# Kernel optimization log

Hardware: AMD Instinct MI355X
Metric: run time of the kernel (lower is better)

## Reference

```python
import jax, jax.numpy as jnp
import numpy as np

USER = 100000
ITEM = 50000
N = USER + ITEM
LATDIM = 64
IMG_DIM = 1024
E_ADJ = 3_000_000
E_IMG = 1_000_000
GNN_LAYERS = 2
RIS_LAMBDA = 1.0
EPS = 1e-12


def spmm(rows, cols, vals, x):
    # sparse [N,N] @ dense [N,D] via gather + segment-sum
    return jax.ops.segment_sum(vals[:, None] * x[cols], rows, num_segments=N)


def setup_inputs() -> dict:
    key = jax.random.key(0)
    ks = jax.random.split(key, 10)
    return {
        "adj_rows": jax.random.randint(ks[0], (E_ADJ,), 0, N, dtype=jnp.int32),
        "adj_cols": jax.random.randint(ks[1], (E_ADJ,), 0, N, dtype=jnp.int32),
        "adj_vals": jax.random.uniform(ks[2], (E_ADJ,), dtype=jnp.float32),
        "img_rows": jax.random.randint(ks[3], (E_IMG,), 0, N, dtype=jnp.int32),
        "img_cols": jax.random.randint(ks[4], (E_IMG,), 0, N, dtype=jnp.int32),
        "img_vals": jax.random.uniform(ks[5], (E_IMG,), dtype=jnp.float32),
        "image_embedding": jax.random.normal(ks[6], (ITEM, IMG_DIM), dtype=jnp.float32),
        "uEmbeds": jax.random.normal(ks[7], (USER, LATDIM), dtype=jnp.float32) * 0.01,
        "iEmbeds": jax.random.normal(ks[8], (ITEM, LATDIM), dtype=jnp.float32) * 0.01,
        "W_trans": jax.random.normal(ks[9], (IMG_DIM, LATDIM), dtype=jnp.float32) * (1.0 / np.sqrt(IMG_DIM)),
        "b_trans": jnp.zeros((LATDIM,), dtype=jnp.float32),
    }


def reference(adj_rows, adj_cols, adj_vals, img_rows, img_cols, img_vals,
              image_embedding, uEmbeds, iEmbeds, W_trans, b_trans):
    # trans == 1: Linear projection of image features
    image_feats = image_embedding @ W_trans + b_trans  # [ITEM, LATDIM]

    # image_adj @ concat(u, i)
    embeds_img_adj = spmm(img_rows, img_cols, img_vals, jnp.concatenate([uEmbeds, iEmbeds], axis=0))

    # F.normalize(image_feats) along dim=1 (L2, eps=1e-12)
    nrm = jnp.linalg.norm(image_feats, axis=1, keepdims=True)
    feats_n = image_feats / jnp.maximum(nrm, EPS)

    embeds_image = spmm(adj_rows, adj_cols, adj_vals, jnp.concatenate([uEmbeds, feats_n], axis=0))
    embeds_image_ = spmm(adj_rows, adj_cols, adj_vals,
                         jnp.concatenate([embeds_image[:USER], iEmbeds], axis=0))
    embeds_image = embeds_image + embeds_image_ + RIS_LAMBDA * embeds_img_adj

    # stacked GCN layers with sum over all layer outputs (including input)
    acc = embeds_image
    cur = embeds_image
    for _ in range(GNN_LAYERS):
        cur = spmm(adj_rows, adj_cols, adj_vals, cur)
        acc = acc + cur

    return acc[:USER], acc[USER:]
```

## Files before the change

### kernel.cpp

```cpp
#include <hip/hip_runtime.h>
#include <hip/hip_fp16.h>

#define USER_N 100000
#define ITEM_N 50000
#define NN (USER_N + ITEM_N)
#define D 64
#define IMGD 1024
#define LDP 68
#define KSPLIT 4
#define KQ (IMGD / KSPLIT)

#define BUCKET_BITS 10
#define BROWS (1 << BUCKET_BITS)
#define NBUCK ((NN + BROWS - 1) >> BUCKET_BITS)
#define CHUNK 4096

typedef _Float16 v4h __attribute__((ext_vector_type(4)));
typedef _Float16 v8h __attribute__((ext_vector_type(8)));
typedef float v4f __attribute__((ext_vector_type(4)));

typedef __attribute__((address_space(1))) unsigned int GU32;
typedef __attribute__((address_space(3))) unsigned int LU32;

__global__ __launch_bounds__(256) void wt_prep(
    const float* __restrict__ W, _Float16* __restrict__ Wt16)
{
    const int id = blockIdx.x * 256 + threadIdx.x;
    if (id >= D * IMGD) return;
    const int c = id >> 10;
    const int k = id & 1023;
    Wt16[id] = (_Float16)W[(size_t)k * D + c];
}

__global__ __launch_bounds__(256) void gemm_mfma7(
    const float* __restrict__ A, const _Float16* __restrict__ Wt16,
    float* __restrict__ P0, float* __restrict__ P123)
{
    __shared__ float As[32 * KQ];
    const int t = threadIdx.x;
    const int w = t >> 6;
    const int lane = t & 63;
    const int l16 = lane & 15;
    const int g = lane >> 4;
    const int tile = blockIdx.x >> 2;
    const int ks = blockIdx.x & 3;
    const int row0 = tile * 32;
    const int kbase = ks * KQ;

#pragma unroll
    for (int i = 0; i < 8; i++) {
        const int r = w * 8 + i;
        const int grow = row0 + r;
        const int garow = grow < ITEM_N ? grow : ITEM_N - 1;
        const int xm = (r & 7) << 4;
        const char* src = reinterpret_cast<const char*>(
            A + (size_t)garow * IMGD + kbase) + ((lane * 16) ^ xm);
        __builtin_amdgcn_global_load_lds(
            (GU32*)src, (LU32*)&As[r * KQ], 16, 0, 0);
    }
    asm volatile("s_waitcnt vmcnt(0)" ::: "memory");
    __syncthreads();

    const int wr = (w >> 1) * 16;
    const int wc = (w & 1) * 32;
    const int rr = wr + l16;
    const char* rbase = reinterpret_cast<const char*>(&As[rr * KQ]);
    const int xm = (rr & 7) << 4;

    v4f acc[2] = {};
    const _Float16* wb = Wt16 + (size_t)l16 * IMGD + kbase + g * 4;

    for (int c = 0; c < KQ; c += 64) {
        const int cb = c * 4;
        const float4 f0 = *reinterpret_cast<const float4*>(rbase + ((cb + g * 16) ^ xm));
        const float4 f1 = *reinterpret_cast<const float4*>(rbase + ((cb + 64 + g * 16) ^ xm));
        const float4 f2 = *reinterpret_cast<const float4*>(rbase + ((cb + 128 + g * 16) ^ xm));
        const float4 f3 = *reinterpret_cast<const float4*>(rbase + ((cb + 192 + g * 16) ^ xm));
        union { v8h v; v4h h[2]; } af0, af1;
        {
            v4h h;
            h[0] = (_Float16)f0.x; h[1] = (_Float16)f0.y;
            h[2] = (_Float16)f0.z; h[3] = (_Float16)f0.w;
            af0.h[0] = h;
            h[0] = (_Float16)f1.x; h[1] = (_Float16)f1.y;
            h[2] = (_Float16)f1.z; h[3] = (_Float16)f1.w;
            af0.h[1] = h;
            h[0] = (_Float16)f2.x; h[1] = (_Float16)f2.y;
            h[2] = (_Float16)f2.z; h[3] = (_Float16)f2.w;
            af1.h[0] = h;
            h[0] = (_Float16)f3.x; h[1] = (_Float16)f3.y;
            h[2] = (_Float16)f3.z; h[3] = (_Float16)f3.w;
            af1.h[1] = h;
        }
#pragma unroll
        for (int n = 0; n < 2; n++) {
            const _Float16* wp = wb + (size_t)(wc + n * 16) * IMGD + c;
            union { v8h v; v4h h[2]; } bf;
            bf.h[0] = *reinterpret_cast<const v4h*>(wp);
            bf.h[1] = *reinterpret_cast<const v4h*>(wp + 16);
            acc[n] = __builtin_amdgcn_mfma_f32_16x16x32_f16(af0.v, bf.v, acc[n], 0, 0, 0);
            bf.h[0] = *reinterpret_cast<const v4h*>(wp + 32);
            bf.h[1] = *reinterpret_cast<const v4h*>(wp + 48);
            acc[n] = __builtin_amdgcn_mfma_f32_16x16x32_f16(af1.v, bf.v, acc[n], 0, 0, 0);
        }
    }
    float* Cp = (ks == 0) ? P0 : P123 + (size_t)(ks - 1) * ITEM_N * D;
#pragma unroll
    for (int n = 0; n < 2; n++) {
        const int col = wc + n * 16 + l16;
#pragma unroll
        for (int r = 0; r < 4; r++) {
            const int grow = row0 + wr + g * 4 + r;
            if (grow < ITEM_N)
                Cp[(size_t)grow * D + col] = acc[n][r];
        }
    }
}

__global__ __launch_bounds__(256) void gemm_feats32(
    const float* __restrict__ A, const float* __restrict__ W,
    const float* __restrict__ b, float* __restrict__ C)
{
    __shared__ float As[32][LDP];
    __shared__ float Ws[64][LDP];
    const int row0 = blockIdx.x * 32;
    const int t = threadIdx.x;
    const int tx = t & 15, ty = t >> 4;
    float acc[2][4] = {};

    const int lr = t >> 4;
    const int lk = (t & 15) * 4;

    for (int k0 = 0; k0 < IMGD; k0 += 64) {
#pragma unroll
        for (int i = 0; i < 2; i++) {
            const int r = lr + i * 16;
            const int grow = row0 + r;
            float4 v = make_float4(0.f, 0.f, 0.f, 0.f);
            if (grow < ITEM_N)
                v = *reinterpret_cast<const float4*>(&A[(size_t)grow * IMGD + k0 + lk]);
            *reinterpret_cast<float4*>(&As[r][lk]) = v;
        }
#pragma unroll
        for (int i = 0; i < 4; i++) {
            const int kr = lr + i * 16;
            float4 v = *reinterpret_cast<const float4*>(&W[(size_t)(k0 + kr) * D + lk]);
            *reinterpret_cast<float4*>(&Ws[kr][lk]) = v;
        }
        __syncthreads();
#pragma unroll
        for (int kb = 0; kb < 16; kb++) {
            float a_[2][4], w_[4][4];
#pragma unroll
            for (int i = 0; i < 2; i++) {
                const float4 v = *reinterpret_cast<const float4*>(&As[ty * 2 + i][kb * 4]);
                a_[i][0] = v.x; a_[i][1] = v.y; a_[i][2] = v.z; a_[i][3] = v.w;
            }
#pragma unroll
            for (int j = 0; j < 4; j++) {
                const float4 v = *reinterpret_cast<const float4*>(&Ws[kb * 4 + j][tx * 4]);
                w_[j][0] = v.x; w_[j][1] = v.y; w_[j][2] = v.z; w_[j][3] = v.w;
            }
#pragma unroll
            for (int j = 0; j < 4; j++)
#pragma unroll
                for (int i = 0; i < 2; i++)
#pragma unroll
                    for (int c = 0; c < 4; c++)
                        acc[i][c] += a_[i][j] * w_[j][c];
        }
        __syncthreads();
    }
    const float4 bias = *reinterpret_cast<const float4*>(&b[tx * 4]);
#pragma unroll
    for (int i = 0; i < 2; i++) {
        const int grow = row0 + ty * 2 + i;
        if (grow < ITEM_N) {
            float4 v;
            v.x = acc[i][0] + bias.x;
            v.y = acc[i][1] + bias.y;
            v.z = acc[i][2] + bias.z;
            v.w = acc[i][3] + bias.w;
            *reinterpret_cast<float4*>(&C[(size_t)grow * D + tx * 4]) = v;
        }
    }
}

__global__ __launch_bounds__(256) void rownorm_h4(
    const float* __restrict__ P0, const float* __restrict__ P123,
    const float* __restrict__ b, __half* __restrict__ Y, int nrows)
{
    const int gid = blockIdx.x * blockDim.x + threadIdx.x;
    const int row = gid >> 6;
    const int lane = threadIdx.x & 63;
    if (row >= nrows) return;
    const size_t idx = (size_t)row * D + lane;
    const size_t N1 = (size_t)ITEM_N * D;
    float v = P0[idx] + P123[idx] + P123[idx + N1] + P123[idx + 2 * N1] + b[lane];
    float s = v * v;
#pragma unroll
    for (int o = 32; o > 0; o >>= 1) s += __shfl_xor(s, o, 64);
    const float scale = 1.0f / fmaxf(sqrtf(s), 1e-12f);
    Y[idx] = __float2half(v * scale);
}

__global__ __launch_bounds__(256) void rownorm(float* __restrict__ X, int nrows)
{
    const int gid = blockIdx.x * blockDim.x + threadIdx.x;
    const int row = gid >> 6;
    const int lane = threadIdx.x & 63;
    if (row >= nrows) return;
    float v = X[(size_t)row * D + lane];
    float s = v * v;
#pragma unroll
    for (int o = 32; o > 0; o >>= 1) s += __shfl_xor(s, o, 64);
    const float scale = 1.0f / fmaxf(sqrtf(s), 1e-12f);
    X[(size_t)row * D + lane] = v * scale;
}

__global__ __launch_bounds__(256) void cvt_x0(
    const float* __restrict__ uE, const float* __restrict__ iE,
    __half* __restrict__ x0, __half* __restrict__ xBI)
{
    const int i = blockIdx.x * 256 + threadIdx.x;
    const int n4u = USER_N * D / 4;
    const int n4 = NN * D / 4;
    if (i >= n4) return;
    const float4 v = (i < n4u) ? reinterpret_cast<const float4*>(uE)[i]
                               : reinterpret_cast<const float4*>(iE)[i - n4u];
    union { uint2 u2; __half2 h[2]; } o;
    o.h[0] = __floats2half2_rn(v.x, v.y);
    o.h[1] = __floats2half2_rn(v.z, v.w);
    *reinterpret_cast<uint2*>(x0 + (size_t)i * 4) = o.u2;
    if (i >= n4u)
        *reinterpret_cast<uint2*>(xBI + (size_t)(i - n4u) * 4) = o.u2;
}

__global__ __launch_bounds__(256) void bucket_count(
    const int* __restrict__ rows, int nnz, int nb, int* __restrict__ histT)
{
    __shared__ int cnt[NBUCK];
    for (int i = threadIdx.x; i < NBUCK; i += 256) cnt[i] = 0;
    __syncthreads();
    const int e0 = blockIdx.x * CHUNK;
    const int e1 = min(e0 + CHUNK, nnz);
    for (int e = e0 + threadIdx.x; e < e1; e += 256)
        atomicAdd(&cnt[rows[e] >> BUCKET_BITS], 1);
    __syncthreads();
    for (int b = threadIdx.x; b < NBUCK; b += 256)
        histT[b * nb + blockIdx.x] = cnt[b];
}

__global__ __launch_bounds__(1024) void scanA(
    const int* __restrict__ cnt, int* __restrict__ excl,
    int* __restrict__ blocksums, int n)
{
    const int t = threadIdx.x;
    const int gid = blockIdx.x * 1024 + t;
    const int lane = t & 63, wid = t >> 6;
    int v = (gid < n) ? cnt[gid] : 0;
    int x = v;
#pragma unroll
    for (int o = 1; o < 64; o <<= 1) {
        int y = __shfl_up(x, o, 64);
        if (lane >= o) x += y;
    }
    __shared__ int ws[16];
    __shared__ int wo[16];
    if (lane == 63) ws[wid] = x;
    __syncthreads();
    if (t < 16) {
        int s = ws[t];
        int xx = s;
#pragma unroll
        for (int o = 1; o < 16; o <<= 1) {
            int y = __shfl_up(xx, o, 16);
            if (t >= o) xx += y;
        }
        wo[t] = xx - s;
        if (t == 15) blocksums[blockIdx.x] = xx;
    }
    __syncthreads();
    if (gid < n) excl[gid] = x - v + wo[wid];
}

__global__ __launch_bounds__(1024) void scanB(int* __restrict__ bs, int nb)
{
    const int t = threadIdx.x;
    const int lane = t & 63, wid = t >> 6;
    int v = (t < nb) ? bs[t] : 0;
    int x = v;
#pragma unroll
    for (int o = 1; o < 64; o <<= 1) {
        int y = __shfl_up(x, o, 64);
        if (lane >= o) x += y;
    }
    __shared__ int ws[16];
    __shared__ int wo[16];
    if (lane == 63) ws[wid] = x;
    __syncthreads();
    if (t < 16) {
        int s = ws[t];
        int xx = s;
#pragma unroll
        for (int o = 1; o < 16; o <<= 1) {
            int y = __shfl_up(xx, o, 16);
            if (t >= o) xx += y;
        }
        wo[t] = xx - s;
    }
    __syncthreads();
    if (t < nb) bs[t] = x - v + wo[wid];
}

__global__ __launch_bounds__(256) void scan_apply(
    int* __restrict__ excl, const int* __restrict__ bo, int n)
{
    const int gid = blockIdx.x * blockDim.x + threadIdx.x;
    if (gid < n) excl[gid] += bo[gid >> 10];
}

__global__ __launch_bounds__(256) void bucket_place(
    const int* __restrict__ rows, const int* __restrict__ cols,
    const float* __restrict__ vals, int nnz, int nb,
    const int* __restrict__ offsT, uint2* __restrict__ rec)
{
    __shared__ int cur[NBUCK];
    for (int b = threadIdx.x; b < NBUCK; b += 256)
        cur[b] = offsT[b * nb + blockIdx.x];
    __syncthreads();
    const int e0 = blockIdx.x * CHUNK;
    const int e1 = min(e0 + CHUNK, nnz);
    for (int e = e0 + threadIdx.x; e < e1; e += 256) {
        const int r = rows[e];
        const int b = r >> BUCKET_BITS;
        const int pos = atomicAdd(&cur[b], 1);
        rec[pos] = make_uint2(((unsigned)cols[e] << BUCKET_BITS) |
                                  (unsigned)(r & (BROWS - 1)),
                              __float_as_uint(vals[e]));
    }
}

__global__ __launch_bounds__(1024) void bucket_finalize(
    const uint2* __restrict__ rec, int nnz, int nb,
    const int* __restrict__ offsT, int* __restrict__ rp,
    int2* __restrict__ ev)
{
    const int b = blockIdx.x;
    const int t = threadIdx.x;
    const int rlo = b << BUCKET_BITS;
    const int segs = offsT[b * nb];
    const int sege = (b + 1 < NBUCK) ? offsT[(b + 1) * nb] : nnz;

    __shared__ int cnt[BROWS];
    __shared__ int cur[BROWS];
    cnt[t] = 0;
    __syncthreads();
    for (int i = segs + t; i < sege; i += 1024)
        atomicAdd(&cnt[rec[i].x & (BROWS - 1)], 1);
    __syncthreads();

    const int lane = t & 63, wid = t >> 6;
    const int v = cnt[t];
    int x = v;
#pragma unroll
    for (int o = 1; o < 64; o <<= 1) {
        int y = __shfl_up(x, o, 64);
        if (lane >= o) x += y;
    }
    __shared__ int wsum[16];
    __shared__ int woff[16];
    if (lane == 63) wsum[wid] = x;
    __syncthreads();
    if (t < 16) {
        int s = wsum[t];
        int xx = s;
#pragma unroll
        for (int o = 1; o < 16; o <<= 1) {
            int y = __shfl_up(xx, o, 16);
            if (t >= o) xx += y;
        }
        woff[t] = xx - s;
    }
    __syncthreads();
    const int start = segs + (x - v + woff[wid]);

    if (rlo + t < NN) rp[rlo + t] = start;
    if (b == NBUCK - 1 && t == 0) rp[NN] = nnz;
    cur[t] = start;
    __syncthreads();

    for (int i = segs + t; i < sege; i += 1024) {
        const uint2 R = rec[i];
        const int rl = (int)(R.x & (BROWS - 1));
        const int c = (int)(R.x >> BUCKET_BITS);
        const int pos = atomicAdd(&cur[rl], 1);
        ev[pos] = make_int2(c, (int)R.y);
    }
}

__global__ __launch_bounds__(256) void spmm_h8(
    const int* __restrict__ rp, const int2* __restrict__ ev,
    const __half* __restrict__ src,
    float* __restrict__ out32, __half* __restrict__ out16, int limit16,
    const float* __restrict__ add1, const float* __restrict__ add2)
{
    const int wid = (blockIdx.x * 256 + threadIdx.x) >> 6;
    const int lane = threadIdx.x & 63;
    const int sub = lane >> 3;
    const int l8 = lane & 7;
    const int rowbase = wid * 8;
    if (rowbase >= NN) return;
    const int row = rowbase + sub;

    int v = 0;
    if (lane <= 8 && rowbase + lane <= NN) v = rp[rowbase + lane];
    const int s = __shfl(v, sub, 64);
    const int e = __shfl(v, sub + 1, 64);

    const __half* srcl = src + l8 * 8;
    float acc[8] = {};

    union cvt4 { uint4 u; __half2 h[4]; };
    int i = s;
    for (; i + 3 < e; i += 4) {
        const int2 E0 = ev[i], E1 = ev[i + 1], E2 = ev[i + 2], E3 = ev[i + 3];
        cvt4 g0, g1, g2, g3;
        g0.u = *reinterpret_cast<const uint4*>(srcl + (size_t)E0.x * D);
        g1.u = *reinterpret_cast<const uint4*>(srcl + (size_t)E1.x * D);
        g2.u = *reinterpret_cast<const uint4*>(srcl + (size_t)E2.x * D);
        g3.u = *reinterpret_cast<const uint4*>(srcl + (size_t)E3.x * D);
#pragma unroll
        for (int k = 0; k < 4; k++) {
            const cvt4& g = k == 0 ? g0 : k == 1 ? g1 : k == 2 ? g2 : g3;
            const float w = __int_as_float(k == 0 ? E0.y : k == 1 ? E1.y
                                           : k == 2 ? E2.y : E3.y);
#pragma unroll
            for (int j = 0; j < 4; j++) {
                const float2 f = __half22float2(g.h[j]);
                acc[2 * j]     += w * f.x;
                acc[2 * j + 1] += w * f.y;
            }
        }
    }
    for (; i < e; i++) {
        const int2 E0 = ev[i];
        cvt4 g;
        g.u = *reinterpret_cast<const uint4*>(srcl + (size_t)E0.x * D);
        const float w = __int_as_float(E0.y);
#pragma unroll
        for (int j = 0; j < 4; j++) {
            const float2 f = __half22float2(g.h[j]);
            acc[2 * j]     += w * f.x;
            acc[2 * j + 1] += w * f.y;
        }
    }

    if (row >= NN) return;
    const size_t idx = (size_t)row * D + l8 * 8;
#pragma unroll
    for (int h = 0; h < 2; h++) {
        if (add1) {
            const float4 a = *reinterpret_cast<const float4*>(&add1[idx + h * 4]);
            acc[4 * h] += a.x; acc[4 * h + 1] += a.y;
            acc[4 * h + 2] += a.z; acc[4 * h + 3] += a.w;
        }
        if (add2) {
            const float4 a = *reinterpret_cast<const float4*>(&add2[idx + h * 4]);
            acc[4 * h] += a.x; acc[4 * h + 1] += a.y;
            acc[4 * h + 2] += a.z; acc[4 * h + 3] += a.w;
        }
        float4 o;
        o.x = acc[4 * h]; o.y = acc[4 * h + 1];
        o.z = acc[4 * h + 2]; o.w = acc[4 * h + 3];
        *reinterpret_cast<float4*>(&out32[idx + h * 4]) = o;
    }
    if (row < limit16) {
        cvt4 o16;
#pragma unroll
        for (int j = 0; j < 4; j++)
            o16.h[j] = __floats2half2_rn(acc[2 * j], acc[2 * j + 1]);
        *reinterpret_cast<uint4*>(&out16[idx]) = o16.u;
    }
}

__global__ __launch_bounds__(256) void spmm_csr(
    const int* __restrict__ rp, const int2* __restrict__ ev,
    const float* __restrict__ srcU, const float* __restrict__ srcI,
    float* __restrict__ out,
    const float* __restrict__ add1, const float* __restrict__ add2)
{
    const int gid = blockIdx.x * blockDim.x + threadIdx.x;
    const int row = gid >> 6;
    const int lane = threadIdx.x & 63;
    if (row >= NN) return;
    const int s = rp[row], e = rp[row + 1];
    float acc = 0.f;
    int i = s;
    for (; i + 3 < e; i += 4) {
        const int2 e0 = ev[i], e1 = ev[i + 1], e2 = ev[i + 2], e3 = ev[i + 3];
        const float* p0 = (e0.x < USER_N) ? (srcU + (size_t)e0.x * D)
                                          : (srcI + (size_t)(e0.x - USER_N) * D);
        const float* p1 = (e1.x < USER_N) ? (srcU + (size_t)e1.x * D)
                                          : (srcI + (size_t)(e1.x - USER_N) * D);
        const float* p2 = (e2.x < USER_N) ? (srcU + (size_t)e2.x * D)
                                          : (srcI + (size_t)(e2.x - USER_N) * D);
        const float* p3 = (e3.x < USER_N) ? (srcU + (size_t)e3.x * D)
                                          : (srcI + (size_t)(e3.x - USER_N) * D);
        acc += __int_as_float(e0.y) * p0[lane];
        acc += __int_as_float(e1.y) * p1[lane];
        acc += __int_as_float(e2.y) * p2[lane];
        acc += __int_as_float(e3.y) * p3[lane];
    }
    for (; i < e; i++) {
        const int2 e0 = ev[i];
        const float* p0 = (e0.x < USER_N) ? (srcU + (size_t)e0.x * D)
                                          : (srcI + (size_t)(e0.x - USER_N) * D);
        acc += __int_as_float(e0.y) * p0[lane];
    }
    const size_t idx = (size_t)row * D + lane;
    if (add1) acc += add1[idx];
    if (add2) acc += add2[idx];
    out[idx] = acc;
}

extern "C" void kernel_launch(void* const* d_in, const int* in_sizes, int n_in,
                              void* d_out, int out_size, void* d_ws, size_t ws_size,
                              hipStream_t stream)
{
    const int*   adj_rows = (const int*)d_in[0];
    const int*   adj_cols = (const int*)d_in[1];
    const float* adj_vals = (const float*)d_in[2];
    const int*   img_rows = (const int*)d_in[3];
    const int*   img_cols = (const int*)d_in[4];
    const float* img_vals = (const float*)d_in[5];
    const float* img_emb  = (const float*)d_in[6];
    const float* uEmb     = (const float*)d_in[7];
    const float* iEmb     = (const float*)d_in[8];
    const float* Wt       = (const float*)d_in[9];
    const float* bt       = (const float*)d_in[10];
    float* out = (float*)d_out;

    const int e_adj = in_sizes[0];
    const int e_img = in_sizes[3];
    const int e_max = e_adj > e_img ? e_adj : e_img;
    const int NB_adj = (e_adj + CHUNK - 1) / CHUNK;
    const int NB_img = (e_img + CHUNK - 1) / CHUNK;
    const int NB_max = NB_adj > NB_img ? NB_adj : NB_img;

    const size_t ndbytes = (size_t)NN * D * sizeof(float);
    const size_t nhbytes = (size_t)NN * D * sizeof(__half);

    size_t off = 0;
    auto carve = [&](size_t bytes) { size_t p = off; off += (bytes + 255) & ~(size_t)255; return p; };
    char* base = (char*)d_ws;
    const size_t o_featsN = carve((size_t)ITEM_N * D * sizeof(float));
    const size_t o_bufA   = carve(ndbytes);
    const size_t o_bufB   = carve(ndbytes);
    const size_t o_rpAdj  = carve((NN + 1) * sizeof(int));
    const size_t o_rpImg  = carve((NN + 1) * sizeof(int));
    const size_t o_bsums  = carve(1024 * sizeof(int));
    const size_t o_histT  = carve((size_t)NBUCK * NB_max * sizeof(int));
    const size_t o_rec    = carve((size_t)e_max * sizeof(uint2) > nhbytes
                                      ? (size_t)e_max * sizeof(uint2) : nhbytes);
    const size_t o_evAdj  = carve((size_t)e_adj * sizeof(int2));
    const size_t need_base = off;
    const size_t o_evImg  = carve((size_t)e_img * sizeof(int2) > nhbytes
                                      ? (size_t)e_img * sizeof(int2) : nhbytes);
    const size_t o_x0     = carve(nhbytes);
    const size_t o_wt16   = carve((size_t)D * IMGD * sizeof(_Float16));
    const size_t need_h = off;

    if (ws_size < need_base) return;
    const bool use_h = (ws_size >= need_h);

    float* featsN = (float*)(base + o_featsN);
    float* bufA   = (float*)(base + o_bufA);
    float* bufB   = (float*)(base + o_bufB);
    int* rpAdj    = (int*)(base + o_rpAdj);
    int* rpImg    = (int*)(base + o_rpImg);
    int* bsums    = (int*)(base + o_bsums);
    int* histT    = (int*)(base + o_histT);
    uint2* rec    = (uint2*)(base + o_rec);
    int2* evAdj   = (int2*)(base + o_evAdj);
    int2* evImg   = (int2*)(base + o_evImg);
    __half* xC    = (__half*)(base + o_rec);
    __half* xB    = (__half*)(base + o_evImg);
    __half* x0    = (__half*)(base + o_x0);
    _Float16* wt16 = (_Float16*)(base + o_wt16);

    {
        const int n = NBUCK * NB_adj;
        const int nsb = (n + 1023) / 1024;
        bucket_count<<<NB_adj, 256, 0, stream>>>(adj_rows, e_adj, NB_adj, histT);
        scanA<<<nsb, 1024, 0, stream>>>(histT, histT, bsums, n);
        scanB<<<1, 1024, 0, stream>>>(bsums, nsb);
        scan_apply<<<(n + 255) / 256, 256, 0, stream>>>(histT, bsums, n);
        bucket_place<<<NB_adj, 256, 0, stream>>>(
            adj_rows, adj_cols, adj_vals, e_adj, NB_adj, histT, rec);
        bucket_finalize<<<NBUCK, 1024, 0, stream>>>(
            rec, e_adj, NB_adj, histT, rpAdj, evAdj);
    }
    {
        const int n = NBUCK * NB_img;
        const int nsb = (n + 1023) / 1024;
        bucket_count<<<NB_img, 256, 0, stream>>>(img_rows, e_img, NB_img, histT);
        scanA<<<nsb, 1024, 0, stream>>>(histT, histT, bsums, n);
        scanB<<<1, 1024, 0, stream>>>(bsums, nsb);
        scan_apply<<<(n + 255) / 256, 256, 0, stream>>>(histT, bsums, n);
        bucket_place<<<NB_img, 256, 0, stream>>>(
            img_rows, img_cols, img_vals, e_img, NB_img, histT, rec);
        bucket_finalize<<<NBUCK, 1024, 0, stream>>>(
            rec, e_img, NB_img, histT, rpImg, evImg);
    }

    const int SPMM8_GRID = (NN + 31) / 32;
    const int SPMM_GRID = (NN * 64 + 255) / 256;
    const int RN_GRID = (ITEM_N * 64 + 255) / 256;
    const int GEMM7_GRID = ((ITEM_N + 31) / 32) * KSPLIT;

    if (use_h) {
        __half* x0I = x0 + (size_t)USER_N * D;
        __half* xBI = xB + (size_t)USER_N * D;

        cvt_x0<<<(NN * D / 4 + 255) / 256, 256, 0, stream>>>(uEmb, iEmb, x0, xBI);

        spmm_h8<<<SPMM8_GRID, 256, 0, stream>>>(
            rpImg, evImg, x0, bufA, nullptr, 0, nullptr, nullptr);

        wt_prep<<<(D * IMGD + 255) / 256, 256, 0, stream>>>(Wt, wt16);
        gemm_mfma7<<<GEMM7_GRID, 256, 0, stream>>>(img_emb, wt16, featsN, bufB);
        rownorm_h4<<<RN_GRID, 256, 0, stream>>>(featsN, bufB, bt, x0I, ITEM_N);

        spmm_h8<<<SPMM8_GRID, 256, 0, stream>>>(
            rpAdj, evAdj, x0, bufB, xB, USER_N, nullptr, nullptr);

        spmm_h8<<<SPMM8_GRID, 256, 0, stream>>>(
            rpAdj, evAdj, xB, bufA, xC, NN, bufB, bufA);

        spmm_h8<<<SPMM8_GRID, 256, 0, stream>>>(
            rpAdj, evAdj, xC, bufB, x0, NN, nullptr, nullptr);

        spmm_h8<<<SPMM8_GRID, 256, 0, stream>>>(
            rpAdj, evAdj, x0, out, nullptr, 0, bufA, bufB);
    } else {
        gemm_feats32<<<(ITEM_N + 31) / 32, 256, 0, stream>>>(img_emb, Wt, bt, featsN);
        rownorm<<<RN_GRID, 256, 0, stream>>>(featsN, ITEM_N);

        spmm_csr<<<SPMM_GRID, 256, 0, stream>>>(
            rpImg, evImg, uEmb, iEmb, bufA, nullptr, nullptr);
        spmm_csr<<<SPMM_GRID, 256, 0, stream>>>(
            rpAdj, evAdj, uEmb, featsN, bufB, nullptr, nullptr);
        spmm_csr<<<SPMM_GRID, 256, 0, stream>>>(
            rpAdj, evAdj, bufB, iEmb, bufA, bufB, bufA);
        spmm_csr<<<SPMM_GRID, 256, 0, stream>>>(
            rpAdj, evAdj, bufA, bufA + (size_t)USER_N * D, bufB, nullptr, nullptr);
        spmm_csr<<<SPMM_GRID, 256, 0, stream>>>(
            rpAdj, evAdj, bufB, bufB + (size_t)USER_N * D, out, bufA, bufB);
    }
}
```

Before: 582.6 us.

## Merge adj/img bucketing launches and co-schedule GEMM with image SpMM

Adjacency and image-adjacency CSR builds now share combined count/place/finalize launches, using separate histogram and record buffers so both run in one grid. The fp16 conversion and weight transpose are fused into one prep kernel. The image SpMM runs as extra blocks inside the MFMA GEMM launch so the two independent jobs overlap. The intent is fewer launches and better device fill, at the cost of more workspace, buffer aliasing (recB reuses the x0 region) and a heterogeneous kernel whose LDS use now also applies to the SpMM blocks.

```diff
diff --git a/kernel.cpp b/kernel.cpp
--- a/kernel.cpp
+++ b/kernel.cpp
@@ -22,97 +22,180 @@
 typedef __attribute__((address_space(1))) unsigned int GU32;
 typedef __attribute__((address_space(3))) unsigned int LU32;
 
-__global__ __launch_bounds__(256) void wt_prep(
-    const float* __restrict__ W, _Float16* __restrict__ Wt16)
-{
-    const int id = blockIdx.x * 256 + threadIdx.x;
-    if (id >= D * IMGD) return;
-    const int c = id >> 10;
-    const int k = id & 1023;
-    Wt16[id] = (_Float16)W[(size_t)k * D + c];
-}
-
-__global__ __launch_bounds__(256) void gemm_mfma7(
+__global__ __launch_bounds__(256) void prep_fused(
+    const float* __restrict__ uE, const float* __restrict__ iE,
+    __half* __restrict__ x0, __half* __restrict__ xBI,
+    const float* __restrict__ W, _Float16* __restrict__ Wt16, int cvt_blocks)
+{
+    if (blockIdx.x < cvt_blocks) {
+        const int i = blockIdx.x * 256 + threadIdx.x;
+        const int n4u = USER_N * D / 4;
+        const int n4 = NN * D / 4;
+        if (i >= n4) return;
+        const float4 v = (i < n4u) ? reinterpret_cast<const float4*>(uE)[i]
+                                   : reinterpret_cast<const float4*>(iE)[i - n4u];
+        union { uint2 u2; __half2 h[2]; } o;
+        o.h[0] = __floats2half2_rn(v.x, v.y);
+        o.h[1] = __floats2half2_rn(v.z, v.w);
+        *reinterpret_cast<uint2*>(x0 + (size_t)i * 4) = o.u2;
+        if (i >= n4u)
+            *reinterpret_cast<uint2*>(xBI + (size_t)(i - n4u) * 4) = o.u2;
+    } else {
+        const int id = (blockIdx.x - cvt_blocks) * 256 + threadIdx.x;
+        if (id >= D * IMGD) return;
+        const int c = id >> 10;
+        const int k = id & 1023;
+        Wt16[id] = (_Float16)W[(size_t)k * D + c];
+    }
+}
+
+__global__ __launch_bounds__(256) void gemm_g(
     const float* __restrict__ A, const _Float16* __restrict__ Wt16,
-    float* __restrict__ P0, float* __restrict__ P123)
+    float* __restrict__ P0, float* __restrict__ P123,
+    const int* __restrict__ rp, const int2* __restrict__ ev,
+    const __half* __restrict__ src, float* __restrict__ out32,
+    int gemm_blocks)
 {
     __shared__ float As[32 * KQ];
-    const int t = threadIdx.x;
-    const int w = t >> 6;
-    const int lane = t & 63;
-    const int l16 = lane & 15;
-    const int g = lane >> 4;
-    const int tile = blockIdx.x >> 2;
-    const int ks = blockIdx.x & 3;
-    const int row0 = tile * 32;
-    const int kbase = ks * KQ;
-
-#pragma unroll
-    for (int i = 0; i < 8; i++) {
-        const int r = w * 8 + i;
-        const int grow = row0 + r;
-        const int garow = grow < ITEM_N ? grow : ITEM_N - 1;
-        const int xm = (r & 7) << 4;
-        const char* src = reinterpret_cast<const char*>(
-            A + (size_t)garow * IMGD + kbase) + ((lane * 16) ^ xm);
-        __builtin_amdgcn_global_load_lds(
-            (GU32*)src, (LU32*)&As[r * KQ], 16, 0, 0);
-    }
-    asm volatile("s_waitcnt vmcnt(0)" ::: "memory");
-    __syncthreads();
-
-    const int wr = (w >> 1) * 16;
-    const int wc = (w & 1) * 32;
-    const int rr = wr + l16;
-    const char* rbase = reinterpret_cast<const char*>(&As[rr * KQ]);
-    const int xm = (rr & 7) << 4;
-
-    v4f acc[2] = {};
-    const _Float16* wb = Wt16 + (size_t)l16 * IMGD + kbase + g * 4;
-
-    for (int c = 0; c < KQ; c += 64) {
-        const int cb = c * 4;
-        const float4 f0 = *reinterpret_cast<const float4*>(rbase + ((cb + g * 16) ^ xm));
-        const float4 f1 = *reinterpret_cast<const float4*>(rbase + ((cb + 64 + g * 16) ^ xm));
-        const float4 f2 = *reinterpret_cast<const float4*>(rbase + ((cb + 128 + g * 16) ^ xm));
-        const float4 f3 = *reinterpret_cast<const float4*>(rbase + ((cb + 192 + g * 16) ^ xm));
-        union { v8h v; v4h h[2]; } af0, af1;
-        {
-            v4h h;
-            h[0] = (_Float16)f0.x; h[1] = (_Float16)f0.y;
-            h[2] = (_Float16)f0.z; h[3] = (_Float16)f0.w;
-            af0.h[0] = h;
-            h[0] = (_Float16)f1.x; h[1] = (_Float16)f1.y;
-            h[2] = (_Float16)f1.z; h[3] = (_Float16)f1.w;
-            af0.h[1] = h;
-            h[0] = (_Float16)f2.x; h[1] = (_Float16)f2.y;
-            h[2] = (_Float16)f2.z; h[3] = (_Float16)f2.w;
-            af1.h[0] = h;
-            h[0] = (_Float16)f3.x; h[1] = (_Float16)f3.y;
-            h[2] = (_Float16)f3.z; h[3] = (_Float16)f3.w;
-            af1.h[1] = h;
-        }
+    if (blockIdx.x < gemm_blocks) {
+        const int t = threadIdx.x;
+        const int w = t >> 6;
+        const int lane = t & 63;
+        const int l16 = lane & 15;
+        const int g = lane >> 4;
+        const int tile = blockIdx.x >> 2;
+        const int ks = blockIdx.x & 3;
+        const int row0 = tile * 32;
+        const int kbase = ks * KQ;
+
+#pragma unroll
+        for (int i = 0; i < 8; i++) {
+            const int r = w * 8 + i;
+            const int grow = row0 + r;
+            const int garow = grow < ITEM_N ? grow : ITEM_N - 1;
+            const int xm = (r & 7) << 4;
+            const char* srcp = reinterpret_cast<const char*>(
+                A + (size_t)garow * IMGD + kbase) + ((lane * 16) ^ xm);
+            __builtin_amdgcn_global_load_lds(
+                (GU32*)srcp, (LU32*)&As[r * KQ], 16, 0, 0);
+        }
+        asm volatile("s_waitcnt vmcnt(0)" ::: "memory");
+        __syncthreads();
+
+        const int wr = (w >> 1) * 16;
+        const int wc = (w & 1) * 32;
+        const int rr = wr + l16;
+        const char* rbase = reinterpret_cast<const char*>(&As[rr * KQ]);
+        const int xm = (rr & 7) << 4;
+
+        v4f acc[2] = {};
+        const _Float16* wb = Wt16 + (size_t)l16 * IMGD + kbase + g * 4;
+
+        for (int c = 0; c < KQ; c += 64) {
+            const int cb = c * 4;
+            const float4 f0 = *reinterpret_cast<const float4*>(rbase + ((cb + g * 16) ^ xm));
+            const float4 f1 = *reinterpret_cast<const float4*>(rbase + ((cb + 64 + g * 16) ^ xm));
+            const float4 f2 = *reinterpret_cast<const float4*>(rbase + ((cb + 128 + g * 16) ^ xm));
+            const float4 f3 = *reinterpret_cast<const float4*>(rbase + ((cb + 192 + g * 16) ^ xm));
+            union { v8h v; v4h h[2]; } af0, af1;
+            {
+                v4h h;
+                h[0] = (_Float16)f0.x; h[1] = (_Float16)f0.y;
+                h[2] = (_Float16)f0.z; h[3] = (_Float16)f0.w;
+                af0.h[0] = h;
+                h[0] = (_Float16)f1.x; h[1] = (_Float16)f1.y;
+                h[2] = (_Float16)f1.z; h[3] = (_Float16)f1.w;
+                af0.h[1] = h;
+                h[0] = (_Float16)f2.x; h[1] = (_Float16)f2.y;
+                h[2] = (_Float16)f2.z; h[3] = (_Float16)f2.w;
+                af1.h[0] = h;
+                h[0] = (_Float16)f3.x; h[1] = (_Float16)f3.y;
+                h[2] = (_Float16)f3.z; h[3] = (_Float16)f3.w;
+                af1.h[1] = h;
+            }
+#pragma unroll
+            for (int n = 0; n < 2; n++) {
+                const _Float16* wp = wb + (size_t)(wc + n * 16) * IMGD + c;
+                union { v8h v; v4h h[2]; } bf;
+                bf.h[0] = *reinterpret_cast<const v4h*>(wp);
+                bf.h[1] = *reinterpret_cast<const v4h*>(wp + 16);
+                acc[n] = __builtin_amdgcn_mfma_f32_16x16x32_f16(af0.v, bf.v, acc[n], 0, 0, 0);
+                bf.h[0] = *reinterpret_cast<const v4h*>(wp + 32);
+                bf.h[1] = *reinterpret_cast<const v4h*>(wp + 48);
+                acc[n] = __builtin_amdgcn_mfma_f32_16x16x32_f16(af1.v, bf.v, acc[n], 0, 0, 0);
+            }
+        }
+        float* Cp = (ks == 0) ? P0 : P123 + (size_t)(ks - 1) * ITEM_N * D;
 #pragma unroll
         for (int n = 0; n < 2; n++) {
-            const _Float16* wp = wb + (size_t)(wc + n * 16) * IMGD + c;
-            union { v8h v; v4h h[2]; } bf;
-            bf.h[0] = *reinterpret_cast<const v4h*>(wp);
-            bf.h[1] = *reinterpret_cast<const v4h*>(wp + 16);
-            acc[n] = __builtin_amdgcn_mfma_f32_16x16x32_f16(af0.v, bf.v, acc[n], 0, 0, 0);
-            bf.h[0] = *reinterpret_cast<const v4h*>(wp + 32);
-            bf.h[1] = *reinterpret_cast<const v4h*>(wp + 48);
-            acc[n] = __builtin_amdgcn_mfma_f32_16x16x32_f16(af1.v, bf.v, acc[n], 0, 0, 0);
-        }
-    }
-    float* Cp = (ks == 0) ? P0 : P123 + (size_t)(ks - 1) * ITEM_N * D;
-#pragma unroll
-    for (int n = 0; n < 2; n++) {
-        const int col = wc + n * 16 + l16;
-#pragma unroll
-        for (int r = 0; r < 4; r++) {
-            const int grow = row0 + wr + g * 4 + r;
-            if (grow < ITEM_N)
-                Cp[(size_t)grow * D + col] = acc[n][r];
+            const int col = wc + n * 16 + l16;
+#pragma unroll
+            for (int r = 0; r < 4; r++) {
+                const int grow = row0 + wr + g * 4 + r;
+                if (grow < ITEM_N)
+                    Cp[(size_t)grow * D + col] = acc[n][r];
+            }
+        }
+    } else {
+        const int wid = ((blockIdx.x - gemm_blocks) * 256 + threadIdx.x) >> 6;
+        const int lane = threadIdx.x & 63;
+        const int sub = lane >> 3;
+        const int l8 = lane & 7;
+        const int rowbase = wid * 8;
+        if (rowbase >= NN) return;
+        const int row = rowbase + sub;
+
+        int v = 0;
+        if (lane <= 8 && rowbase + lane <= NN) v = rp[rowbase + lane];
+        const int s = __shfl(v, sub, 64);
+        const int e = __shfl(v, sub + 1, 64);
+
+        const __half* srcl = src + l8 * 8;
+        float acc[8] = {};
+
+        union cvt4 { uint4 u; __half2 h[4]; };
+        int i = s;
+        for (; i + 3 < e; i += 4) {
+            const int2 E0 = ev[i], E1 = ev[i + 1], E2 = ev[i + 2], E3 = ev[i + 3];
+            cvt4 g0, g1, g2, g3;
+            g0.u = *reinterpret_cast<const uint4*>(srcl + (size_t)E0.x * D);
+            g1.u = *reinterpret_cast<const uint4*>(srcl + (size_t)E1.x * D);
+            g2.u = *reinterpret_cast<const uint4*>(srcl + (size_t)E2.x * D);
+            g3.u = *reinterpret_cast<const uint4*>(srcl + (size_t)E3.x * D);
+#pragma unroll
+            for (int k = 0; k < 4; k++) {
+                const cvt4& g = k == 0 ? g0 : k == 1 ? g1 : k == 2 ? g2 : g3;
+                const float w = __int_as_float(k == 0 ? E0.y : k == 1 ? E1.y
+                                               : k == 2 ? E2.y : E3.y);
+#pragma unroll
+                for (int j = 0; j < 4; j++) {
+                    const float2 f = __half22float2(g.h[j]);
+                    acc[2 * j]     += w * f.x;
+                    acc[2 * j + 1] += w * f.y;
+                }
+            }
+        }
+        for (; i < e; i++) {
+            const int2 E0 = ev[i];
+            cvt4 g;
+            g.u = *reinterpret_cast<const uint4*>(srcl + (size_t)E0.x * D);
+            const float w = __int_as_float(E0.y);
+#pragma unroll
+            for (int j = 0; j < 4; j++) {
+                const float2 f = __half22float2(g.h[j]);
+                acc[2 * j]     += w * f.x;
+                acc[2 * j + 1] += w * f.y;
+            }
+        }
+
+        if (row >= NN) return;
+        const size_t idx = (size_t)row * D + l8 * 8;
+#pragma unroll
+        for (int h = 0; h < 2; h++) {
+            float4 o;
+            o.x = acc[4 * h]; o.y = acc[4 * h + 1];
+            o.z = acc[4 * h + 2]; o.w = acc[4 * h + 3];
+            *reinterpret_cast<float4*>(&out32[idx + h * 4]) = o;
         }
     }
 }
@@ -218,37 +301,27 @@
     X[(size_t)row * D + lane] = v * scale;
 }
 
-__global__ __launch_bounds__(256) void cvt_x0(
-    const float* __restrict__ uE, const float* __restrict__ iE,
-    __half* __restrict__ x0, __half* __restrict__ xBI)
-{
-    const int i = blockIdx.x * 256 + threadIdx.x;
-    const int n4u = USER_N * D / 4;
-    const int n4 = NN * D / 4;
-    if (i >= n4) return;
-    const float4 v = (i < n4u) ? reinterpret_cast<const float4*>(uE)[i]
-                               : reinterpret_cast<const float4*>(iE)[i - n4u];
-    union { uint2 u2; __half2 h[2]; } o;
-    o.h[0] = __floats2half2_rn(v.x, v.y);
-    o.h[1] = __floats2half2_rn(v.z, v.w);
-    *reinterpret_cast<uint2*>(x0 + (size_t)i * 4) = o.u2;
-    if (i >= n4u)
-        *reinterpret_cast<uint2*>(xBI + (size_t)(i - n4u) * 4) = o.u2;
-}
-
-__global__ __launch_bounds__(256) void bucket_count(
-    const int* __restrict__ rows, int nnz, int nb, int* __restrict__ histT)
-{
+__global__ __launch_bounds__(256) void bucket_count2(
+    const int* __restrict__ rows_a, int nnz_a, int nb_a, int* __restrict__ histT_a,
+    const int* __restrict__ rows_b, int nnz_b, int nb_b, int* __restrict__ histT_b)
+{
+    const bool isA = (int)blockIdx.x < nb_a;
+    const int bid = isA ? blockIdx.x : blockIdx.x - nb_a;
+    const int* rows = isA ? rows_a : rows_b;
+    const int nnz = isA ? nnz_a : nnz_b;
+    const int nb = isA ? nb_a : nb_b;
+    int* histT = isA ? histT_a : histT_b;
+
     __shared__ int cnt[NBUCK];
     for (int i = threadIdx.x; i < NBUCK; i += 256) cnt[i] = 0;
     __syncthreads();
-    const int e0 = blockIdx.x * CHUNK;
+    const int e0 = bid * CHUNK;
     const int e1 = min(e0 + CHUNK, nnz);
     for (int e = e0 + threadIdx.x; e < e1; e += 256)
         atomicAdd(&cnt[rows[e] >> BUCKET_BITS], 1);
     __syncthreads();
     for (int b = threadIdx.x; b < NBUCK; b += 256)
-        histT[b * nb + blockIdx.x] = cnt[b];
+        histT[b * nb + bid] = cnt[b];
 }
 
 __global__ __launch_bounds__(1024) void scanA(
@@ -320,16 +393,29 @@
     if (gid < n) excl[gid] += bo[gid >> 10];
 }
 
-__global__ __launch_bounds__(256) void bucket_place(
-    const int* __restrict__ rows, const int* __restrict__ cols,
-    const float* __restrict__ vals, int nnz, int nb,
-    const int* __restrict__ offsT, uint2* __restrict__ rec)
-{
+__global__ __launch_bounds__(256) void bucket_place2(
+    const int* __restrict__ rows_a, const int* __restrict__ cols_a,
+    const float* __restrict__ vals_a, int nnz_a, int nb_a,
+    const int* __restrict__ offsT_a, uint2* __restrict__ rec_a,
+    const int* __restrict__ rows_b, const int* __restrict__ cols_b,
+    const float* __restrict__ vals_b, int nnz_b, int nb_b,
+    const int* __restrict__ offsT_b, uint2* __restrict__ rec_b)
+{
+    const bool isA = (int)blockIdx.x < nb_a;
+    const int bid = isA ? blockIdx.x : blockIdx.x - nb_a;
+    const int* rows = isA ? rows_a : rows_b;
+    const int* cols = isA ? cols_a : cols_b;
+    const float* vals = isA ? vals_a : vals_b;
+    const int nnz = isA ? nnz_a : nnz_b;
+    const int nb = isA ? nb_a : nb_b;
+    const int* offsT = isA ? offsT_a : offsT_b;
+    uint2* rec = isA ? rec_a : rec_b;
+
     __shared__ int cur[NBUCK];
     for (int b = threadIdx.x; b < NBUCK; b += 256)
-        cur[b] = offsT[b * nb + blockIdx.x];
-    __syncthreads();
-    const int e0 = blockIdx.x * CHUNK;
+        cur[b] = offsT[b * nb + bid];
+    __syncthreads();
+    const int e0 = bid * CHUNK;
     const int e1 = min(e0 + CHUNK, nnz);
     for (int e = e0 + threadIdx.x; e < e1; e += 256) {
         const int r = rows[e];
@@ -341,12 +427,21 @@
     }
 }
 
-__global__ __launch_bounds__(1024) void bucket_finalize(
-    const uint2* __restrict__ rec, int nnz, int nb,
-    const int* __restrict__ offsT, int* __restrict__ rp,
-    int2* __restrict__ ev)
-{
-    const int b = blockIdx.x;
+__global__ __launch_bounds__(1024) void bucket_finalize2(
+    const uint2* __restrict__ rec_a, int nnz_a, int nb_a,
+    const int* __restrict__ offsT_a, int* __restrict__ rp_a, int2* __restrict__ ev_a,
+    const uint2* __restrict__ rec_b, int nnz_b, int nb_b,
+    const int* __restrict__ offsT_b, int* __restrict__ rp_b, int2* __restrict__ ev_b)
+{
+    const bool isA = (int)blockIdx.x < NBUCK;
+    const int b = isA ? blockIdx.x : blockIdx.x - NBUCK;
+    const uint2* rec = isA ? rec_a : rec_b;
+    const int nnz = isA ? nnz_a : nnz_b;
+    const int nb = isA ? nb_a : nb_b;
+    const int* offsT = isA ? offsT_a : offsT_b;
+    int* rp = isA ? rp_a : rp_b;
+    int2* ev = isA ? ev_a : ev_b;
+
     const int t = threadIdx.x;
     const int rlo = b << BUCKET_BITS;
     const int segs = offsT[b * nb];
@@ -546,7 +641,6 @@
     const int e_max = e_adj > e_img ? e_adj : e_img;
     const int NB_adj = (e_adj + CHUNK - 1) / CHUNK;
     const int NB_img = (e_img + CHUNK - 1) / CHUNK;
-    const int NB_max = NB_adj > NB_img ? NB_adj : NB_img;
 
     const size_t ndbytes = (size_t)NN * D * sizeof(float);
     const size_t nhbytes = (size_t)NN * D * sizeof(__half);
@@ -560,14 +654,16 @@
     const size_t o_rpAdj  = carve((NN + 1) * sizeof(int));
     const size_t o_rpImg  = carve((NN + 1) * sizeof(int));
     const size_t o_bsums  = carve(1024 * sizeof(int));
-    const size_t o_histT  = carve((size_t)NBUCK * NB_max * sizeof(int));
-    const size_t o_rec    = carve((size_t)e_max * sizeof(uint2) > nhbytes
+    const size_t o_histTA = carve((size_t)NBUCK * NB_adj * sizeof(int));
+    const size_t o_histTB = carve((size_t)NBUCK * NB_img * sizeof(int));
+    const size_t o_recA   = carve((size_t)e_max * sizeof(uint2) > nhbytes
                                       ? (size_t)e_max * sizeof(uint2) : nhbytes);
     const size_t o_evAdj  = carve((size_t)e_adj * sizeof(int2));
     const size_t need_base = off;
     const size_t o_evImg  = carve((size_t)e_img * sizeof(int2) > nhbytes
                                       ? (size_t)e_img * sizeof(int2) : nhbytes);
-    const size_t o_x0     = carve(nhbytes);
+    const size_t o_x0     = carve((size_t)e_img * sizeof(uint2) > nhbytes
+                                      ? (size_t)e_img * sizeof(uint2) : nhbytes);
     const size_t o_wt16   = carve((size_t)D * IMGD * sizeof(_Float16));
     const size_t need_h = off;
 
@@ -580,56 +676,52 @@
     int* rpAdj    = (int*)(base + o_rpAdj);
     int* rpImg    = (int*)(base + o_rpImg);
     int* bsums    = (int*)(base + o_bsums);
-    int* histT    = (int*)(base + o_histT);
-    uint2* rec    = (uint2*)(base + o_rec);
+    int* histTA   = (int*)(base + o_histTA);
+    int* histTB   = (int*)(base + o_histTB);
+    uint2* recA   = (uint2*)(base + o_recA);
+    uint2* recB   = (uint2*)(base + o_x0);
     int2* evAdj   = (int2*)(base + o_evAdj);
     int2* evImg   = (int2*)(base + o_evImg);
-    __half* xC    = (__half*)(base + o_rec);
+    __half* xC    = (__half*)(base + o_recA);
     __half* xB    = (__half*)(base + o_evImg);
     __half* x0    = (__half*)(base + o_x0);
     _Float16* wt16 = (_Float16*)(base + o_wt16);
 
-    {
-        const int n = NBUCK * NB_adj;
-        const int nsb = (n + 1023) / 1024;
-        bucket_count<<<NB_adj, 256, 0, stream>>>(adj_rows, e_adj, NB_adj, histT);
-        scanA<<<nsb, 1024, 0, stream>>>(histT, histT, bsums, n);
-        scanB<<<1, 1024, 0, stream>>>(bsums, nsb);
-        scan_apply<<<(n + 255) / 256, 256, 0, stream>>>(histT, bsums, n);
-        bucket_place<<<NB_adj, 256, 0, stream>>>(
-            adj_rows, adj_cols, adj_vals, e_adj, NB_adj, histT, rec);
-        bucket_finalize<<<NBUCK, 1024, 0, stream>>>(
-            rec, e_adj, NB_adj, histT, rpAdj, evAdj);
-    }
-    {
-        const int n = NBUCK * NB_img;
-        const int nsb = (n + 1023) / 1024;
-        bucket_count<<<NB_img, 256, 0, stream>>>(img_rows, e_img, NB_img, histT);
-        scanA<<<nsb, 1024, 0, stream>>>(histT, histT, bsums, n);
-        scanB<<<1, 1024, 0, stream>>>(bsums, nsb);
-        scan_apply<<<(n + 255) / 256, 256, 0, stream>>>(histT, bsums, n);
-        bucket_place<<<NB_img, 256, 0, stream>>>(
-            img_rows, img_cols, img_vals, e_img, NB_img, histT, rec);
-        bucket_finalize<<<NBUCK, 1024, 0, stream>>>(
-            rec, e_img, NB_img, histT, rpImg, evImg);
-    }
-
     const int SPMM8_GRID = (NN + 31) / 32;
     const int SPMM_GRID = (NN * 64 + 255) / 256;
     const int RN_GRID = (ITEM_N * 64 + 255) / 256;
-    const int GEMM7_GRID = ((ITEM_N + 31) / 32) * KSPLIT;
+    const int GEMM_BLOCKS = ((ITEM_N + 31) / 32) * KSPLIT;
 
     if (use_h) {
         __half* x0I = x0 + (size_t)USER_N * D;
         __half* xBI = xB + (size_t)USER_N * D;
 
-        cvt_x0<<<(NN * D / 4 + 255) / 256, 256, 0, stream>>>(uEmb, iEmb, x0, xBI);
-
-        spmm_h8<<<SPMM8_GRID, 256, 0, stream>>>(
-            rpImg, evImg, x0, bufA, nullptr, 0, nullptr, nullptr);
-
-        wt_prep<<<(D * IMGD + 255) / 256, 256, 0, stream>>>(Wt, wt16);
-        gemm_mfma7<<<GEMM7_GRID, 256, 0, stream>>>(img_emb, wt16, featsN, bufB);
+        bucket_count2<<<NB_adj + NB_img, 256, 0, stream>>>(
+            adj_rows, e_adj, NB_adj, histTA, img_rows, e_img, NB_img, histTB);
+        {
+            const int nA = NBUCK * NB_adj, nsbA = (nA + 1023) / 1024;
+            scanA<<<nsbA, 1024, 0, stream>>>(histTA, histTA, bsums, nA);
+            scanB<<<1, 1024, 0, stream>>>(bsums, nsbA);
+            scan_apply<<<(nA + 255) / 256, 256, 0, stream>>>(histTA, bsums, nA);
+            const int nB = NBUCK * NB_img, nsbB = (nB + 1023) / 1024;
+            scanA<<<nsbB, 1024, 0, stream>>>(histTB, histTB, bsums, nB);
+            scanB<<<1, 1024, 0, stream>>>(bsums, nsbB);
+            scan_apply<<<(nB + 255) / 256, 256, 0, stream>>>(histTB, bsums, nB);
+        }
+        bucket_place2<<<NB_adj + NB_img, 256, 0, stream>>>(
+            adj_rows, adj_cols, adj_vals, e_adj, NB_adj, histTA, recA,
+            img_rows, img_cols, img_vals, e_img, NB_img, histTB, recB);
+        bucket_finalize2<<<2 * NBUCK, 1024, 0, stream>>>(
+            recA, e_adj, NB_adj, histTA, rpAdj, evAdj,
+            recB, e_img, NB_img, histTB, rpImg, evImg);
+
+        const int CVT_BLOCKS = (NN * D / 4 + 255) / 256;
+        prep_fused<<<CVT_BLOCKS + (D * IMGD + 255) / 256, 256, 0, stream>>>(
+            uEmb, iEmb, x0, xBI, Wt, wt16, CVT_BLOCKS);
+
+        gemm_g<<<GEMM_BLOCKS + SPMM8_GRID, 256, 0, stream>>>(
+            img_emb, wt16, featsN, bufB, rpImg, evImg, x0, bufA, GEMM_BLOCKS);
+
         rownorm_h4<<<RN_GRID, 256, 0, stream>>>(featsN, bufB, bt, x0I, ITEM_N);
 
         spmm_h8<<<SPMM8_GRID, 256, 0, stream>>>(
@@ -644,6 +736,25 @@
         spmm_h8<<<SPMM8_GRID, 256, 0, stream>>>(
             rpAdj, evAdj, x0, out, nullptr, 0, bufA, bufB);
     } else {
+        bucket_count2<<<NB_adj + NB_img, 256, 0, stream>>>(
+            adj_rows, e_adj, NB_adj, histTA, img_rows, e_img, NB_img, histTB);
+        {
+            const int nA = NBUCK * NB_adj, nsbA = (nA + 1023) / 1024;
+            scanA<<<nsbA, 1024, 0, stream>>>(histTA, histTA, bsums, nA);
+            scanB<<<1, 1024, 0, stream>>>(bsums, nsbA);
+            scan_apply<<<(nA + 255) / 256, 256, 0, stream>>>(histTA, bsums, nA);
+            const int nB = NBUCK * NB_img, nsbB = (nB + 1023) / 1024;
+            scanA<<<nsbB, 1024, 0, stream>>>(histTB, histTB, bsums, nB);
+            scanB<<<1, 1024, 0, stream>>>(bsums, nsbB);
+            scan_apply<<<(nB + 255) / 256, 256, 0, stream>>>(histTB, bsums, nB);
+        }
+        bucket_place2<<<NB_adj + NB_img, 256, 0, stream>>>(
+            adj_rows, adj_cols, adj_vals, e_adj, NB_adj, histTA, recA,
+            img_rows, img_cols, img_vals, e_img, NB_img, histTB, recB);
+        bucket_finalize2<<<2 * NBUCK, 1024, 0, stream>>>(
+            recA, e_adj, NB_adj, histTA, rpAdj, evAdj,
+            recB, e_img, NB_img, histTB, rpImg, evImg);
+
         gemm_feats32<<<(ITEM_N + 31) / 32, 256, 0, stream>>>(img_emb, Wt, bt, featsN);
         rownorm<<<RN_GRID, 256, 0, stream>>>(featsN, ITEM_N);
 
```

New measurement: 565.1 us. -3.0%, faster.
